# Kernel optimization log

Measured on AMD Instinct MI355X. Metric: run time of the kernel, lower is better.

The kernel has to match this reference:

```python
import jax, jax.numpy as jnp
import numpy as np

EMBEDDING_BOUND = 1e4  # uniform init bound for box centers (repo constant)


def setup_inputs() -> dict:
    key = jax.random.key(0)
    k1, k2, k3 = jax.random.split(key, 3)
    num_classes, dim = 100000, 50
    d = dim // 2
    # init per MultiBoxEL.init_embeddings: centers ~ U(-B, B), offsets ~ N(1, 0.333)
    centers = jax.random.uniform(k1, (num_classes, d), dtype=jnp.float32,
                                 minval=-EMBEDDING_BOUND, maxval=EMBEDDING_BOUND)
    offsets = 1.0 + 0.333 * jax.random.normal(k2, (num_classes, d), dtype=jnp.float32)
    class_embeds = jnp.concatenate([centers, offsets], axis=1)  # [C, dim]
    nf1_data = jax.random.randint(k3, (2_000_000, 2), 0, num_classes)  # [N, 2] class ids
    return {"class_embeds": class_embeds, "nf1_data": nf1_data}


def _to_box(emb):
    # get_multiboxes: first half = center, second half = |offsets|
    d = emb.shape[-1] // 2
    return emb[:, :d], jnp.abs(emb[:, d:])


def reference(class_embeds, nf1_data):
    """nf1_loss (C subsumed-by D): batched inclusion loss 1 - Area(C ^ D)/Area(C),
    then L2 norm of relu(losses) over the batch (a scalar), exactly as inclusion_loss."""
    c_emb = class_embeds[nf1_data[:, 0]]  # [N, dim] gather (memory-bound)
    d_emb = class_embeds[nf1_data[:, 1]]
    cc, co = _to_box(c_emb)
    dc, do = _to_box(d_emb)
    # box intersection: [max(lowers), min(uppers)]; empty -> side length clipped to 0
    lo = jnp.maximum(cc - co, dc - do)
    hi = jnp.minimum(cc + co, dc + do)
    inter_area = jnp.prod(jax.nn.relu(hi - lo), axis=-1)  # [N]
    c_area = jnp.prod(2.0 * co, axis=-1)                  # [N] box volume = prod(2*offset)
    loss = jnp.where(c_area == 0, 0.0,
           jnp.where(jnp.isinf(c_area), 1.0 - inter_area / (2.0 * EMBEDDING_BOUND),
                     1.0 - inter_area / c_area))
    return jnp.linalg.norm(jax.nn.relu(loss))
```

## Files before the change

### kernel.cpp

```cpp
#include <hip/hip_runtime.h>
#include <math.h>


#define DIMS 25
#define EMB_BOUND 10000.0f
#define FBLK 1024
#define TROWS 128
#define TFLOATS (TROWS * 2 * DIMS)

__global__ void init_ws_kernel(float* ws) {
    if (threadIdx.x == 0 && blockIdx.x == 0) ws[0] = 0.0f;
}

__global__ __launch_bounds__(256, 8) void nf1_fallback_kernel(
    const float* __restrict__ emb, const int2* __restrict__ pairs,
    int n_pairs, float* __restrict__ ws)
{
    const int gl  = threadIdx.x & 31;
    const int gid = blockIdx.x * (blockDim.x >> 5) + (threadIdx.x >> 5);
    const int ngrp = gridDim.x * (blockDim.x >> 5);
    float acc = 0.0f;
    for (int p = gid; p < n_pairs; p += ngrp) {
        int2 pr = pairs[p];
        const float* rc = emb + (size_t)pr.x * (2 * DIMS);
        const float* rd = emb + (size_t)pr.y * (2 * DIMS);
        float t = 1.0f, a = 1.0f;
        if (gl < DIMS) {
            float cc = rc[gl], co = fabsf(rc[DIMS + gl]);
            float dc = rd[gl], dd = fabsf(rd[DIMS + gl]);
            float lo = fmaxf(cc - co, dc - dd);
            float hi = fminf(cc + co, dc + dd);
            t = fmaxf(hi - lo, 0.0f);
            a = 2.0f * co;
        }
        #pragma unroll
        for (int m = 16; m >= 1; m >>= 1) { t *= __shfl_xor(t, m, 32); a *= __shfl_xor(a, m, 32); }
        float loss;
        if (a == 0.0f)     loss = 0.0f;
        else if (isinf(a)) loss = 1.0f - t / (2.0f * EMB_BOUND);
        else               loss = 1.0f - t / a;
        loss = fmaxf(loss, 0.0f);
        if (gl == 0) acc += loss * loss;
    }
    #pragma unroll
    for (int m = 32; m >= 1; m >>= 1) acc += __shfl_xor(acc, m, 64);
    __shared__ float wsum[4];
    if ((threadIdx.x & 63) == 0) wsum[threadIdx.x >> 6] = acc;
    __syncthreads();
    if (threadIdx.x == 0) atomicAdd(ws, wsum[0] + wsum[1] + wsum[2] + wsum[3]);
}

__global__ void fallback_finalize_kernel(const float* __restrict__ ws, float* __restrict__ out) {
    if (threadIdx.x == 0 && blockIdx.x == 0) out[0] = sqrtf(fmaxf(ws[0], 0.0f));
}

__device__ __forceinline__ float slow_pair(const float* __restrict__ emb, int2 pr) {
    const float* ra = emb + (size_t)pr.x * (2 * DIMS);
    const float* rb = emb + (size_t)pr.y * (2 * DIMS);
    float inter = 1.0f, carea = 1.0f;
    for (int j = 0; j < DIMS; j++) {
        float cc = ra[j], co = fabsf(ra[DIMS + j]);
        float dc = rb[j], dd = fabsf(rb[DIMS + j]);
        float lo = fmaxf(cc - co, dc - dd);
        float hi = fminf(cc + co, dc + dd);
        inter *= fmaxf(hi - lo, 0.0f);
        carea *= 2.0f * co;
    }
    float loss;
    if (carea == 0.0f)     loss = 0.0f;
    else if (isinf(carea)) loss = 1.0f - inter / (2.0f * EMB_BOUND);
    else                   loss = 1.0f - inter / carea;
    loss = fmaxf(loss, 0.0f);
    return loss * loss;
}

__device__ __forceinline__ float key_pair(const float2* __restrict__ keys,
                                          const float* __restrict__ emb, int2 pr) {
    float2 ka = keys[pr.x];
    float2 kb = keys[pr.y];
    float t0 = fminf(ka.y, kb.y) - fmaxf(ka.x, kb.x);
    if (t0 > 0.0f) return slow_pair(emb, pr);
    return 1.0f;
}

template <int K>
__device__ __forceinline__ int ring_bucket(float lo, float hi) {
    float w = hi - lo;
    if (w <= 16.0f && fabsf(lo) <= 1.0e6f) {
        int i = (int)floorf(lo * 0.0625f);
        int b = i % K; if (b < 0) b += K;
        return b;
    }
    return K;
}

__device__ __forceinline__ bool ring_pass(unsigned a, unsigned b, unsigned K) {
    unsigned dd = (a >= b) ? (a - b) : (b - a);
    return (a == K) | (b == K) | (dd <= 1u) | (dd == K - 1u);
}

__global__ __launch_bounds__(256) void repack_tile_kernel(
    const float* __restrict__ emb, float2* __restrict__ keys,
    unsigned char* __restrict__ gbuck, int n_rows,
    float* __restrict__ acc, unsigned* __restrict__ ticket)
{
    __shared__ float tile[TFLOATS];
    if (blockIdx.x == 0 && threadIdx.x == 0) { acc[0] = 0.0f; ticket[0] = 0u; }
    const int n_tiles = (n_rows + TROWS - 1) / TROWS;
    for (int tIdx = blockIdx.x; tIdx < n_tiles; tIdx += gridDim.x) {
        const int r0 = tIdx * TROWS;
        const int rows = min(TROWS, n_rows - r0);
        const int cnt = rows * (2 * DIMS);
        const int n4 = cnt >> 2;
        {
            const float4* g4 = (const float4*)(emb + (size_t)r0 * (2 * DIMS));
            float4* s4 = (float4*)tile;
            for (int i = threadIdx.x; i < n4; i += blockDim.x) s4[i] = g4[i];
            for (int i = (n4 << 2) + threadIdx.x; i < cnt; i += blockDim.x)
                tile[i] = emb[(size_t)r0 * (2 * DIMS) + i];
        }
        __syncthreads();
        for (int j = threadIdx.x; j < rows; j += blockDim.x) {
            float c = tile[j * (2 * DIMS)];
            float o = fabsf(tile[j * (2 * DIMS) + DIMS]);
            float lo = c - o, hi = c + o;
            keys[r0 + j] = make_float2(lo, hi);
            gbuck[r0 + j] = (unsigned char)ring_bucket<255>(lo, hi);
        }
        __syncthreads();
    }
}

__global__ __launch_bounds__(FBLK, 1) void screen_byte_kernel(
    const float2* __restrict__ keys, const unsigned char* __restrict__ gbuck,
    const float* __restrict__ emb, const int2* __restrict__ pairs,
    int n_pairs, int n_rows, float* __restrict__ acc,
    unsigned* __restrict__ ticket, float* __restrict__ out)
{
    extern __shared__ unsigned char sbuck[];
    __shared__ float wsum[FBLK / 64];
    const int nthreads = gridDim.x * blockDim.x;
    const int t = blockIdx.x * blockDim.x + threadIdx.x;
    const int noct = n_pairs >> 3;
    const int4* p4 = (const int4*)pairs;

    int4 qa, qb, qc, qd;
    const bool have0 = t < noct;
    if (have0) {
        qa = p4[4 * t + 0]; qb = p4[4 * t + 1];
        qc = p4[4 * t + 2]; qd = p4[4 * t + 3];
    }

    {
        const int nb16 = (n_rows + 15) >> 4;
        const uint4* g4 = (const uint4*)gbuck;
        uint4* s4 = (uint4*)sbuck;
        for (int i = threadIdx.x; i < nb16; i += blockDim.x) s4[i] = g4[i];
    }
    __syncthreads();

    float sum = 0.0f;
    for (int q = t; q < noct; q += nthreads) {
        if (q != t) {
            qa = p4[4 * q + 0]; qb = p4[4 * q + 1];
            qc = p4[4 * q + 2]; qd = p4[4 * q + 3];
        }
        int2 pr[8] = { make_int2(qa.x, qa.y), make_int2(qa.z, qa.w),
                       make_int2(qb.x, qb.y), make_int2(qb.z, qb.w),
                       make_int2(qc.x, qc.y), make_int2(qc.z, qc.w),
                       make_int2(qd.x, qd.y), make_int2(qd.z, qd.w) };
        unsigned ba[8], bb[8];
        #pragma unroll
        for (int i = 0; i < 8; i++) { ba[i] = sbuck[pr[i].x]; bb[i] = sbuck[pr[i].y]; }
        #pragma unroll
        for (int i = 0; i < 8; i++) {
            if (ring_pass(ba[i], bb[i], 255u)) sum += key_pair(keys, emb, pr[i]);
            else                               sum += 1.0f;
        }
    }
    for (int p = (noct << 3) + t; p < n_pairs; p += nthreads) {
        int2 pr = pairs[p];
        unsigned a = sbuck[pr.x], b = sbuck[pr.y];
        if (ring_pass(a, b, 255u)) sum += key_pair(keys, emb, pr);
        else                       sum += 1.0f;
    }

    #pragma unroll
    for (int m = 32; m >= 1; m >>= 1) sum += __shfl_xor(sum, m, 64);
    if ((threadIdx.x & 63) == 0) wsum[threadIdx.x >> 6] = sum;
    __syncthreads();
    if (threadIdx.x == 0) {
        float s = 0.0f;
        #pragma unroll
        for (int w = 0; w < FBLK / 64; w++) s += wsum[w];
        atomicAdd(acc, s);
        __threadfence();
        unsigned tk = atomicAdd(ticket, 1u);
        if (tk == gridDim.x - 1)
            out[0] = sqrtf(fmaxf(atomicAdd(acc, 0.0f), 0.0f));
    }
}

extern "C" void kernel_launch(void* const* d_in, const int* in_sizes, int n_in,
                              void* d_out, int out_size, void* d_ws, size_t ws_size,
                              hipStream_t stream) {
    const float* emb  = (const float*)d_in[0];
    const int2*  prs  = (const int2*)d_in[1];
    int n_pairs = in_sizes[1] / 2;
    int n_rows  = in_sizes[0] / (2 * DIMS);

    float*    ws     = (float*)d_ws;
    unsigned* ticket = (unsigned*)(ws + 1);
    float*    out    = (float*)d_out;
    float2*   keys   = (float2*)((char*)d_ws + 256);
    unsigned char* gbuck = (unsigned char*)(keys + n_rows);


    const size_t tabBytes = (size_t)((n_rows + 15) & ~15);
    const bool byte_ok = (ws_size >= 256 + (size_t)n_rows * 8 + tabBytes + 64) &&
                         ((n_rows & 1) == 0) &&
                         (tabBytes + 512 <= 160 * 1024);

    if (byte_ok) {
        const int n_tiles = (n_rows + TROWS - 1) / TROWS;
        hipLaunchKernelGGL(repack_tile_kernel, dim3(min(n_tiles, 2048)), dim3(256),
                           0, stream, emb, keys, gbuck, n_rows, ws, ticket);
        hipLaunchKernelGGL(screen_byte_kernel, dim3(256), dim3(FBLK),
                           tabBytes, stream,
                           keys, gbuck, emb, prs, n_pairs, n_rows, ws, ticket, out);
    } else {
        hipLaunchKernelGGL(init_ws_kernel, dim3(1), dim3(64), 0, stream, ws);
        hipLaunchKernelGGL(nf1_fallback_kernel, dim3(4096), dim3(256), 0, stream,
                           emb, prs, n_pairs, ws);
        hipLaunchKernelGGL(fallback_finalize_kernel, dim3(1), dim3(64), 0, stream, ws, out);
    }
}
```

Measured before the change: 87.07 us.

## Pack screening buckets as 6-bit codes, five per word, in shared memory

Replaces the byte-per-row bucket table (255 buckets of width 16) with 6-bit codes (63 buckets of width 64) packed five per 32-bit word, shrinking the shared-memory table from about 100KB to about 80KB. The smaller LDS footprint may allow two 1024-thread blocks per CU, and the screen grid doubles to 512 blocks with 4 pairs per iteration instead of 8. In exchange, each lookup needs a divide-by-5 and a shift, and the coarser buckets let more pairs through to the exact key and slow paths.

```diff
diff --git a/kernel.cpp b/kernel.cpp
--- a/kernel.cpp
+++ b/kernel.cpp
@@ -4,8 +4,8 @@
 
 #define DIMS 25
 #define EMB_BOUND 10000.0f
-#define FBLK 1024
-#define TROWS 128
+#define SBLK 1024
+#define TROWS 160
 #define TFLOATS (TROWS * 2 * DIMS)
 
 __global__ void init_ws_kernel(float* ws) {
@@ -83,28 +83,34 @@
     return 1.0f;
 }
 
-template <int K>
-__device__ __forceinline__ int ring_bucket(float lo, float hi) {
+__device__ __forceinline__ unsigned ring_bucket6(float lo, float hi) {
     float w = hi - lo;
-    if (w <= 16.0f && fabsf(lo) <= 1.0e6f) {
-        int i = (int)floorf(lo * 0.0625f);
-        int b = i % K; if (b < 0) b += K;
-        return b;
-    }
-    return K;
-}
-
-__device__ __forceinline__ bool ring_pass(unsigned a, unsigned b, unsigned K) {
+    if (w <= 64.0f && fabsf(lo) <= 1.0e6f) {
+        int i = (int)floorf(lo * 0.015625f);
+        int b = i % 63; if (b < 0) b += 63;
+        return (unsigned)b;
+    }
+    return 63u;
+}
+
+__device__ __forceinline__ unsigned lookup6(const unsigned* __restrict__ tab, int idx) {
+    int w = idx / 5;
+    int r = idx - 5 * w;
+    return (tab[w] >> (6 * r)) & 63u;
+}
+
+__device__ __forceinline__ bool ring_pass6(unsigned a, unsigned b) {
     unsigned dd = (a >= b) ? (a - b) : (b - a);
-    return (a == K) | (b == K) | (dd <= 1u) | (dd == K - 1u);
-}
-
-__global__ __launch_bounds__(256) void repack_tile_kernel(
+    return (a == 63u) | (b == 63u) | (dd <= 1u) | (dd == 62u);
+}
+
+__global__ __launch_bounds__(256) void repack6_kernel(
     const float* __restrict__ emb, float2* __restrict__ keys,
-    unsigned char* __restrict__ gbuck, int n_rows,
+    unsigned* __restrict__ gpack, int n_rows,
     float* __restrict__ acc, unsigned* __restrict__ ticket)
 {
     __shared__ float tile[TFLOATS];
+    __shared__ unsigned char scode[TROWS];
     if (blockIdx.x == 0 && threadIdx.x == 0) { acc[0] = 0.0f; ticket[0] = 0u; }
     const int n_tiles = (n_rows + TROWS - 1) / TROWS;
     for (int tIdx = blockIdx.x; tIdx < n_tiles; tIdx += gridDim.x) {
@@ -125,64 +131,68 @@
             float o = fabsf(tile[j * (2 * DIMS) + DIMS]);
             float lo = c - o, hi = c + o;
             keys[r0 + j] = make_float2(lo, hi);
-            gbuck[r0 + j] = (unsigned char)ring_bucket<255>(lo, hi);
+            scode[j] = (unsigned char)ring_bucket6(lo, hi);
         }
         __syncthreads();
-    }
-}
-
-__global__ __launch_bounds__(FBLK, 1) void screen_byte_kernel(
-    const float2* __restrict__ keys, const unsigned char* __restrict__ gbuck,
+        const int nwords = (rows + 4) / 5;
+        for (int w = threadIdx.x; w < nwords; w += blockDim.x) {
+            unsigned word = 0;
+            #pragma unroll
+            for (int k = 0; k < 5; k++) {
+                int j = 5 * w + k;
+                unsigned c = (j < rows) ? (unsigned)scode[j] : 63u;
+                word |= c << (6 * k);
+            }
+            gpack[r0 / 5 + w] = word;
+        }
+        __syncthreads();
+    }
+}
+
+__global__ __launch_bounds__(SBLK) void screen6_kernel(
+    const float2* __restrict__ keys, const unsigned* __restrict__ gpack,
     const float* __restrict__ emb, const int2* __restrict__ pairs,
     int n_pairs, int n_rows, float* __restrict__ acc,
     unsigned* __restrict__ ticket, float* __restrict__ out)
 {
-    extern __shared__ unsigned char sbuck[];
-    __shared__ float wsum[FBLK / 64];
+    extern __shared__ unsigned stab[];
+    __shared__ float wsum[SBLK / 64];
     const int nthreads = gridDim.x * blockDim.x;
     const int t = blockIdx.x * blockDim.x + threadIdx.x;
-    const int noct = n_pairs >> 3;
+    const int nquad = n_pairs >> 2;
     const int4* p4 = (const int4*)pairs;
 
-    int4 qa, qb, qc, qd;
-    const bool have0 = t < noct;
-    if (have0) {
-        qa = p4[4 * t + 0]; qb = p4[4 * t + 1];
-        qc = p4[4 * t + 2]; qd = p4[4 * t + 3];
-    }
+    int4 q0, q1;
+    if (t < nquad) { q0 = p4[2 * t]; q1 = p4[2 * t + 1]; }
 
     {
-        const int nb16 = (n_rows + 15) >> 4;
-        const uint4* g4 = (const uint4*)gbuck;
-        uint4* s4 = (uint4*)sbuck;
-        for (int i = threadIdx.x; i < nb16; i += blockDim.x) s4[i] = g4[i];
+        const int nwords = (n_rows + 4) / 5;
+        const int n16 = (nwords + 3) >> 2;
+        const uint4* g4 = (const uint4*)gpack;
+        uint4* s4 = (uint4*)stab;
+        for (int i = threadIdx.x; i < n16; i += blockDim.x) s4[i] = g4[i];
     }
     __syncthreads();
 
     float sum = 0.0f;
-    for (int q = t; q < noct; q += nthreads) {
-        if (q != t) {
-            qa = p4[4 * q + 0]; qb = p4[4 * q + 1];
-            qc = p4[4 * q + 2]; qd = p4[4 * q + 3];
-        }
-        int2 pr[8] = { make_int2(qa.x, qa.y), make_int2(qa.z, qa.w),
-                       make_int2(qb.x, qb.y), make_int2(qb.z, qb.w),
-                       make_int2(qc.x, qc.y), make_int2(qc.z, qc.w),
-                       make_int2(qd.x, qd.y), make_int2(qd.z, qd.w) };
-        unsigned ba[8], bb[8];
-        #pragma unroll
-        for (int i = 0; i < 8; i++) { ba[i] = sbuck[pr[i].x]; bb[i] = sbuck[pr[i].y]; }
-        #pragma unroll
-        for (int i = 0; i < 8; i++) {
-            if (ring_pass(ba[i], bb[i], 255u)) sum += key_pair(keys, emb, pr[i]);
-            else                               sum += 1.0f;
-        }
-    }
-    for (int p = (noct << 3) + t; p < n_pairs; p += nthreads) {
+    for (int q = t; q < nquad; q += nthreads) {
+        if (q != t) { q0 = p4[2 * q]; q1 = p4[2 * q + 1]; }
+        int2 pr[4] = { make_int2(q0.x, q0.y), make_int2(q0.z, q0.w),
+                       make_int2(q1.x, q1.y), make_int2(q1.z, q1.w) };
+        unsigned ba[4], bb[4];
+        #pragma unroll
+        for (int i = 0; i < 4; i++) { ba[i] = lookup6(stab, pr[i].x); bb[i] = lookup6(stab, pr[i].y); }
+        #pragma unroll
+        for (int i = 0; i < 4; i++) {
+            if (ring_pass6(ba[i], bb[i])) sum += key_pair(keys, emb, pr[i]);
+            else                          sum += 1.0f;
+        }
+    }
+    for (int p = (nquad << 2) + t; p < n_pairs; p += nthreads) {
         int2 pr = pairs[p];
-        unsigned a = sbuck[pr.x], b = sbuck[pr.y];
-        if (ring_pass(a, b, 255u)) sum += key_pair(keys, emb, pr);
-        else                       sum += 1.0f;
+        unsigned a = lookup6(stab, pr.x), b = lookup6(stab, pr.y);
+        if (ring_pass6(a, b)) sum += key_pair(keys, emb, pr);
+        else                  sum += 1.0f;
     }
 
     #pragma unroll
@@ -192,7 +202,7 @@
     if (threadIdx.x == 0) {
         float s = 0.0f;
         #pragma unroll
-        for (int w = 0; w < FBLK / 64; w++) s += wsum[w];
+        for (int w = 0; w < SBLK / 64; w++) s += wsum[w];
         atomicAdd(acc, s);
         __threadfence();
         unsigned tk = atomicAdd(ticket, 1u);
@@ -213,21 +223,21 @@
     unsigned* ticket = (unsigned*)(ws + 1);
     float*    out    = (float*)d_out;
     float2*   keys   = (float2*)((char*)d_ws + 256);
-    unsigned char* gbuck = (unsigned char*)(keys + n_rows);
-
-
-    const size_t tabBytes = (size_t)((n_rows + 15) & ~15);
-    const bool byte_ok = (ws_size >= 256 + (size_t)n_rows * 8 + tabBytes + 64) &&
-                         ((n_rows & 1) == 0) &&
-                         (tabBytes + 512 <= 160 * 1024);
-
-    if (byte_ok) {
+    unsigned* gpack  = (unsigned*)(keys + n_rows);
+
+    const int    packWords = (n_rows + 4) / 5;
+    const size_t packPad   = ((size_t)packWords * 4 + 15) & ~(size_t)15;
+    const bool ws_ok = (ws_size >= 256 + (size_t)n_rows * 8 + packPad + 64) &&
+                       ((n_rows & 1) == 0);
+    const bool path_ok = ws_ok && (packPad + 512 <= 160 * 1024);
+
+    if (path_ok) {
         const int n_tiles = (n_rows + TROWS - 1) / TROWS;
-        hipLaunchKernelGGL(repack_tile_kernel, dim3(min(n_tiles, 2048)), dim3(256),
-                           0, stream, emb, keys, gbuck, n_rows, ws, ticket);
-        hipLaunchKernelGGL(screen_byte_kernel, dim3(256), dim3(FBLK),
-                           tabBytes, stream,
-                           keys, gbuck, emb, prs, n_pairs, n_rows, ws, ticket, out);
+        hipLaunchKernelGGL(repack6_kernel, dim3(min(n_tiles, 2048)), dim3(256),
+                           0, stream, emb, keys, gpack, n_rows, ws, ticket);
+        hipLaunchKernelGGL(screen6_kernel, dim3(512), dim3(SBLK),
+                           packPad, stream,
+                           keys, gpack, emb, prs, n_pairs, n_rows, ws, ticket, out);
     } else {
         hipLaunchKernelGGL(init_ws_kernel, dim3(1), dim3(64), 0, stream, ws);
         hipLaunchKernelGGL(nf1_fallback_kernel, dim3(4096), dim3(256), 0, stream,
```

Measured after the change: 94.06 us. 1.08x slower.
